# Optimization experiments

Hardware: AMD Instinct MI355X
Metric: run time of the kernel (lower is better)

## Reference

```python
import jax, jax.numpy as jnp
import numpy as np

N, E, H, L, T = 20000, 160000, 128, 4, 20


def _ln(x, g, b):
    m = jnp.mean(x, -1, keepdims=True)
    v = jnp.mean((x - m) ** 2, -1, keepdims=True)
    return (x - m) * jax.lax.rsqrt(v + 1e-5) * g + b


def _mlp(x, W1, b1, W2, b2, g, b):
    # Linear -> ReLU -> Linear -> LayerNorm, as in mlp_2layer
    h = jax.nn.relu(x @ W1 + b1)
    return _ln(h @ W2 + b2, g, b)


def setup_inputs() -> dict:
    key = jax.random.key(0)
    ks = iter(jax.random.split(key, 64))

    def W(shape):
        fan_in = shape[-2]
        return jax.random.normal(next(ks), shape, jnp.float32) * (fan_in ** -0.5)

    z = lambda s: jnp.zeros(s, jnp.float32)
    o = lambda s: jnp.ones(s, jnp.float32)

    inp = {
        'x': jax.random.normal(next(ks), (N, 12), jnp.float32),
        'edge_attr': jax.random.normal(next(ks), (E, 4), jnp.float32),
        'edge_index': jax.random.randint(next(ks), (2, E), 0, N),
        # node encoder (12 -> H)
        'Wn1': W((12, H)), 'bn1': z((H,)), 'Wn2': W((H, H)), 'bn2': z((H,)), 'gn_ln': o((H,)), 'bn_ln': z((H,)),
        # edge encoder (4 -> H)
        'We1': W((4, H)), 'be1': z((H,)), 'We2': W((H, H)), 'be2': z((H,)), 'ge_ln': o((H,)), 'be_ln': z((H,)),
        # stacked per-layer params: edge_mlp (4H -> H), node_mlp (3H -> H), global_mlp (3H -> H)
        'lEW1': W((L, 4 * H, H)), 'lEb1': z((L, H)), 'lEW2': W((L, H, H)), 'lEb2': z((L, H)), 'lEg': o((L, H)), 'lEbt': z((L, H)),
        'lVW1': W((L, 3 * H, H)), 'lVb1': z((L, H)), 'lVW2': W((L, H, H)), 'lVb2': z((L, H)), 'lVg': o((L, H)), 'lVbt': z((L, H)),
        'lGW1': W((L, 3 * H, H)), 'lGb1': z((L, H)), 'lGW2': W((L, H, H)), 'lGb2': z((L, H)), 'lGg': o((L, H)), 'lGbt': z((L, H)),
        # CNN output head: Conv1d(1->8,k=15,s=4) -> ReLU -> Conv1d(8->1,k=10,s=1)
        'c1w': jax.random.normal(next(ks), (8, 1, 15), jnp.float32) * 0.1, 'c1b': z((8,)),
        'c2w': jax.random.normal(next(ks), (1, 8, 10), jnp.float32) * 0.1, 'c2b': z((1,)),
    }
    return inp


def _forward(x, edge_attr, edge_index,
             Wn1, bn1, Wn2, bn2, gn_ln, bn_ln,
             We1, be1, We2, be2, ge_ln, be_ln,
             lEW1, lEb1, lEW2, lEb2, lEg, lEbt,
             lVW1, lVb1, lVW2, lVb2, lVg, lVbt,
             lGW1, lGb1, lGW2, lGb2, lGg, lGbt,
             c1w, c1b, c2w, c2b):
    senders = edge_index[0]
    receivers = edge_index[1]
    n_nodes = x.shape[0]
    n_edges = edge_attr.shape[0]

    x_v = _mlp(x, Wn1, bn1, Wn2, bn2, gn_ln, bn_ln)          # [N, H]
    x_e = _mlp(edge_attr, We1, be1, We2, be2, ge_ln, be_ln)  # [E, H]
    g = jnp.zeros((1, H), x_v.dtype)                          # B=1 global (no global inputs)

    def step(carry, p):
        x_v, x_e, g = carry
        (EW1, Eb1, EW2, Eb2, Eg, Ebt,
         VW1, Vb1, VW2, Vb2, Vg, Vbt,
         GW1, Gb1, GW2, Gb2, Gg, Gbt) = p
        # edge update: gather sender/receiver feats, concat with edge + global
        g_e = jnp.broadcast_to(g, (n_edges, H))
        edge_in = jnp.concatenate([x_v[senders], x_v[receivers], x_e, g_e], -1)  # [E, 4H]
        x_e = x_e + _mlp(edge_in, EW1, Eb1, EW2, Eb2, Eg, Ebt)
        # node update: sum-aggregate messages by receiver
        aggr = jax.ops.segment_sum(x_e, receivers, num_segments=n_nodes)  # [N, H]
        g_v = jnp.broadcast_to(g, (n_nodes, H))
        node_in = jnp.concatenate([x_v, aggr, g_v], -1)  # [N, 3H]
        x_v = x_v + _mlp(node_in, VW1, Vb1, VW2, Vb2, Vg, Vbt)
        # global update
        g_in = jnp.concatenate([jnp.sum(x_v, 0, keepdims=True), jnp.sum(x_e, 0, keepdims=True), g], -1)  # [1, 3H]
        g = g + _mlp(g_in, GW1, Gb1, GW2, Gb2, Gg, Gbt)
        return (x_v, x_e, g), None

    params = (lEW1, lEb1, lEW2, lEb2, lEg, lEbt,
              lVW1, lVb1, lVW2, lVb2, lVg, lVbt,
              lGW1, lGb1, lGW2, lGb2, lGg, lGbt)
    (x_v, x_e, g), _ = jax.lax.scan(step, (x_v, x_e, g), params)

    # CNN head over the H=128 feature axis -> [N, T]
    dn = ('NCH', 'OIH', 'NCH')
    h = x_v[:, None, :]  # [N, 1, 128]
    h = jax.lax.conv_general_dilated(h, c1w, (4,), 'VALID', dimension_numbers=dn)
    h = jax.nn.relu(h + c1b[None, :, None])  # [N, 8, 29]
    h = jax.lax.conv_general_dilated(h, c2w, (1,), 'VALID', dimension_numbers=dn) + c2b[None, :, None]
    return h[:, 0, :]  # [N, 20]


def reference(x, edge_attr, edge_index,
              Wn1, bn1, Wn2, bn2, gn_ln, bn_ln,
              We1, be1, We2, be2, ge_ln, be_ln,
              lEW1, lEb1, lEW2, lEb2, lEg, lEbt,
              lVW1, lVb1, lVW2, lVb2, lVg, lVbt,
              lGW1, lGb1, lGW2, lGb2, lGg, lGbt,
              c1w, c1b, c2w, c2b):
    return _forward(x, edge_attr, edge_index,
                    Wn1, bn1, Wn2, bn2, gn_ln, bn_ln,
                    We1, be1, We2, be2, ge_ln, be_ln,
                    lEW1, lEb1, lEW2, lEb2, lEg, lEbt,
                    lVW1, lVb1, lVW2, lVb2, lVg, lVbt,
                    lGW1, lGb1, lGW2, lGb2, lGg, lGbt,
                    c1w, c1b, c2w, c2b)
```

## Files before the change

kernel.cpp:

```cpp
#include <hip/hip_runtime.h>

#define NN 20000
#define NE 160000
#define HD 128
#define SA 136

typedef __attribute__((ext_vector_type(8))) short  bfrag;
typedef __attribute__((ext_vector_type(4))) short  s4v;
typedef __attribute__((ext_vector_type(4))) float  facc;
typedef __attribute__((ext_vector_type(4))) float  f4v;

__device__ __forceinline__ float bf2f(unsigned short u){
  union { unsigned int i; float f; } v; v.i = ((unsigned int)u) << 16; return v.f;
}
__device__ __forceinline__ unsigned short f2bf(float f){
  union { float f; unsigned int i; } v; v.f = f;
  unsigned int r = v.i + 0x7fffu + ((v.i >> 16) & 1u);
  return (unsigned short)(r >> 16);
}

__global__ void sentinel_kernel(float* out, float code){
  if (threadIdx.x < 32) out[threadIdx.x] = code;
}

__device__ __forceinline__ void gemm_tile(const short* Ab,
                                          const unsigned short* pk,
                                          int m0, int lane, facc acc[8]){
  const int q = lane >> 4, c = lane & 15;
  #pragma unroll
  for (int kt = 0; kt < 4; ++kt){
    bfrag a = *(const bfrag*)(Ab + (m0 + c) * SA + kt * 32 + q * 8);
    const bfrag* bp = (const bfrag*)pk + kt * 512 + lane;
    #pragma unroll
    for (int nt = 0; nt < 8; ++nt){
      acc[nt] = __builtin_amdgcn_mfma_f32_16x16x32_bf16(a, bp[nt * 64], acc[nt], 0, 0, 0);
    }
  }
}

__device__ __forceinline__ void gemm_tile_h(const short* Ab,
                                            const unsigned short* pk,
                                            int m0, int ntb, int lane, facc acc[4]){
  const int q = lane >> 4, c = lane & 15;
  #pragma unroll
  for (int kt = 0; kt < 4; ++kt){
    bfrag a = *(const bfrag*)(Ab + (m0 + c) * SA + kt * 32 + q * 8);
    const bfrag* bp = (const bfrag*)pk + kt * 512 + ntb * 64 + lane;
    #pragma unroll
    for (int nt = 0; nt < 4; ++nt){
      acc[nt] = __builtin_amdgcn_mfma_f32_16x16x32_bf16(a, bp[nt * 64], acc[nt], 0, 0, 0);
    }
  }
}

__global__ __launch_bounds__(256) void pack_all(
    const float* Wn2, const float* We2,
    const float* lEW1, const float* lEW2,
    const float* lVW1, const float* lVW2,
    unsigned short* packed)
{
  int job = blockIdx.x * 256 + threadIdx.x;
  int mat = job >> 12, r12 = job & 4095;
  int plane = r12 >> 11, r = r12 & 2047;
  int kt = r >> 9, nt = (r >> 6) & 7, lane = r & 63;
  const float* src;
  if (mat == 0) src = Wn2;
  else if (mat == 1) src = We2;
  else {
    int m2 = mat - 2, l = m2 / 7, t = m2 % 7;
    switch (t){
      case 0: src = lEW1 + ((size_t)l*512 +   0)*HD; break;
      case 1: src = lEW1 + ((size_t)l*512 + 128)*HD; break;
      case 2: src = lEW1 + ((size_t)l*512 + 256)*HD; break;
      case 3: src = lEW2 + (size_t)l*HD*HD;          break;
      case 4: src = lVW1 + ((size_t)l*384 +   0)*HD; break;
      case 5: src = lVW1 + ((size_t)l*384 + 128)*HD; break;
      default: src = lVW2 + (size_t)l*HD*HD;         break;
    }
  }
  int krow = kt*32 + (lane>>4)*8, col = nt*16 + (lane&15);
  unsigned short v[8];
  #pragma unroll
  for (int j = 0; j < 8; ++j){
    float w = src[(size_t)(krow + j)*HD + col];
    unsigned short h = f2bf(w);
    v[j] = plane ? f2bf(w - bf2f(h)) : h;
  }
  unsigned short* dst = packed + ((size_t)mat*2 + plane)*16384
                               + ((size_t)(kt*8+nt)*64 + lane)*8;
  #pragma unroll
  for (int j = 0; j < 8; ++j) dst[j] = v[j];
}

__global__ __launch_bounds__(128) void init_small(
    float* g, float* cbe, float* cbv, float* xvs, float* xes,
    const float* Eb1_0, const float* Vb1_0)
{
  int t = threadIdx.x;
  g[t] = 0.f; xvs[t] = 0.f; xes[t] = 0.f;
  cbe[t] = Eb1_0[t]; cbv[t] = Vb1_0[t];
}

__global__ __launch_bounds__(256) void zero_cnt(int* cnt){
  int i = blockIdx.x * 256 + threadIdx.x;
  if (i < NN) cnt[i] = 0;
}
__global__ __launch_bounds__(256) void hist_kernel(const int* eidx, int* cnt){
  int e = blockIdx.x * 256 + threadIdx.x;
  atomicAdd(&cnt[eidx[NE + e]], 1);
}
__global__ __launch_bounds__(1024) void scan_kernel(const int* cnt, int* base, int* ofs){
  __shared__ int wsum[16];
  int t = threadIdx.x, lane = t & 63;
  int vals[20]; int loc = 0;
  if (t < 1000){
    #pragma unroll
    for (int k = 0; k < 20; ++k){ vals[k] = cnt[t*20 + k]; loc += vals[k]; }
  }
  int inc = loc;
  #pragma unroll
  for (int d = 1; d < 64; d <<= 1){ int o = __shfl_up(inc, d); if (lane >= d) inc += o; }
  if (lane == 63) wsum[t >> 6] = inc;
  __syncthreads();
  if (t < 16){
    int v = wsum[t];
    #pragma unroll
    for (int d = 1; d < 16; d <<= 1){ int o = __shfl_up(v, d); if (t >= d) v += o; }
    wsum[t] = v;
  }
  __syncthreads();
  int woff = (t >= 64) ? wsum[(t >> 6) - 1] : 0;
  int run = woff + inc - loc;
  if (t < 1000){
    #pragma unroll
    for (int k = 0; k < 20; ++k){ base[t*20 + k] = run; ofs[t*20 + k] = run; run += vals[k]; }
  }
  if (t == 0) base[NN] = NE;
}
__global__ __launch_bounds__(256) void scatter_kernel(const int* eidx, int* ofs,
                                                      int* perm, int* ssid, int* srid){
  int e = blockIdx.x * 256 + threadIdx.x;
  int s = eidx[e], r = eidx[NE + e];
  int pos = atomicAdd(&ofs[r], 1);
  perm[pos] = e; ssid[pos] = s; srid[pos] = r;
}

__global__ __launch_bounds__(256) void enc_node(
    const float* x, const float* W1, const float* b1,
    const unsigned short* pkW2, const float* b2,
    const float* gl, const float* bl, float* xvf, int nrows)
{
  __shared__ float inb[64*12];
  __shared__ __align__(16) short Hh[64*SA];
  __shared__ __align__(16) short Hl[64*SA];
  int tid = threadIdx.x, r0 = blockIdx.x * 64;
  for (int j = tid; j < 64*12; j += 256){
    int rr = j / 12, k = j % 12, rg = r0 + rr;
    inb[j] = (rg < nrows) ? x[(size_t)rg*12 + k] : 0.f;
  }
  __syncthreads();
  {
    int cc = tid & 127;
    float w1c[12];
    #pragma unroll
    for (int k = 0; k < 12; ++k) w1c[k] = W1[k*HD + cc];
    float bb = b1[cc];
    for (int it = 0; it < 32; ++it){
      int rr = it*2 + (tid >> 7);
      float a = bb;
      #pragma unroll
      for (int k = 0; k < 12; ++k) a += inb[rr*12 + k] * w1c[k];
      float h = fmaxf(a, 0.f);
      unsigned short hh = f2bf(h);
      Hh[rr*SA + cc] = (short)hh;
      Hl[rr*SA + cc] = (short)f2bf(h - bf2f(hh));
    }
  }
  __syncthreads();
  int lane = tid & 63, q = lane >> 4, c = lane & 15, m0 = (tid >> 6) * 16;
  facc a2[8];
  #pragma unroll
  for (int nt = 0; nt < 8; ++nt) a2[nt] = (facc){0.f,0.f,0.f,0.f};
  gemm_tile(Hh, pkW2,         m0, lane, a2);
  gemm_tile(Hl, pkW2,         m0, lane, a2);
  gemm_tile(Hh, pkW2 + 16384, m0, lane, a2);
  #pragma unroll
  for (int i = 0; i < 4; ++i){
    int rl = m0 + q*4 + i, rg = r0 + rl;
    float vals[8], s = 0.f, ss = 0.f;
    #pragma unroll
    for (int nt = 0; nt < 8; ++nt){
      float v = a2[nt][i] + b2[nt*16 + c];
      vals[nt] = v; s += v; ss += v*v;
    }
    s += __shfl_xor(s,1); ss += __shfl_xor(ss,1);
    s += __shfl_xor(s,2); ss += __shfl_xor(ss,2);
    s += __shfl_xor(s,4); ss += __shfl_xor(ss,4);
    s += __shfl_xor(s,8); ss += __shfl_xor(ss,8);
    float mean = s * 0.0078125f;
    float var  = ss * 0.0078125f - mean*mean;
    float rs   = rsqrtf(var + 1e-5f);
    if (rg < nrows){
      #pragma unroll
      for (int nt = 0; nt < 8; ++nt){
        int col = nt*16 + c;
        xvf[(size_t)rg*HD + col] = (vals[nt]-mean)*rs*gl[col] + bl[col];
      }
    }
  }
}

__global__ __launch_bounds__(256) void enc_edge(
    const float* ea, const int* perm, const float* W1, const float* b1,
    const unsigned short* pkW2, const float* b2,
    const float* gl, const float* bl, unsigned short* xeb)
{
  __shared__ float inb[64*4];
  __shared__ __align__(16) short Hh[64*SA];
  __shared__ __align__(16) short Hl[64*SA];
  int tid = threadIdx.x, r0 = blockIdx.x * 64;
  {
    int rr = tid >> 2, k = tid & 3;
    int pe = perm[r0 + rr];
    inb[tid] = ea[(size_t)pe*4 + k];
  }
  __syncthreads();
  {
    int cc = tid & 127;
    float w0 = W1[0*HD+cc], w1 = W1[1*HD+cc], w2 = W1[2*HD+cc], w3 = W1[3*HD+cc];
    float bb = b1[cc];
    for (int it = 0; it < 32; ++it){
      int rr = it*2 + (tid >> 7);
      float a = bb + inb[rr*4+0]*w0 + inb[rr*4+1]*w1 + inb[rr*4+2]*w2 + inb[rr*4+3]*w3;
      float h = fmaxf(a, 0.f);
      unsigned short hh = f2bf(h);
      Hh[rr*SA + cc] = (short)hh;
      Hl[rr*SA + cc] = (short)f2bf(h - bf2f(hh));
    }
  }
  __syncthreads();
  int lane = tid & 63, q = lane >> 4, c = lane & 15, m0 = (tid >> 6) * 16;
  facc a2[8];
  #pragma unroll
  for (int nt = 0; nt < 8; ++nt) a2[nt] = (facc){0.f,0.f,0.f,0.f};
  gemm_tile(Hh, pkW2,         m0, lane, a2);
  gemm_tile(Hl, pkW2,         m0, lane, a2);
  gemm_tile(Hh, pkW2 + 16384, m0, lane, a2);
  #pragma unroll
  for (int i = 0; i < 4; ++i){
    int rl = m0 + q*4 + i, rg = r0 + rl;
    float vals[8], s = 0.f, ss = 0.f;
    #pragma unroll
    for (int nt = 0; nt < 8; ++nt){
      float v = a2[nt][i] + b2[nt*16 + c];
      vals[nt] = v; s += v; ss += v*v;
    }
    s += __shfl_xor(s,1); ss += __shfl_xor(ss,1);
    s += __shfl_xor(s,2); ss += __shfl_xor(ss,2);
    s += __shfl_xor(s,4); ss += __shfl_xor(ss,4);
    s += __shfl_xor(s,8); ss += __shfl_xor(ss,8);
    float mean = s * 0.0078125f;
    float var  = ss * 0.0078125f - mean*mean;
    float rs   = rsqrtf(var + 1e-5f);
    #pragma unroll
    for (int nt = 0; nt < 8; ++nt){
      int col = nt*16 + c;
      xeb[(size_t)rg*HD + col] = f2bf((vals[nt]-mean)*rs*gl[col] + bl[col]);
    }
  }
}

__global__ __launch_bounds__(512, 4) void pq_kernel(
    const float* xvf, const unsigned short* pkA, const unsigned short* pkB,
    unsigned short* P, unsigned short* Q, int nrows)
{
  __shared__ __align__(16) short Ah[64*SA];
  __shared__ __align__(16) short Al[64*SA];
  int tid = threadIdx.x, r0 = blockIdx.x * 64;
  for (int j = tid; j < 1024; j += 512){
    int rr = j >> 4, ch = j & 15, rg = r0 + rr;
    float v[8];
    if (rg < nrows){
      f4v a = *(const f4v*)(xvf + (size_t)rg*HD + ch*8);
      f4v b = *(const f4v*)(xvf + (size_t)rg*HD + ch*8 + 4);
      v[0]=a[0];v[1]=a[1];v[2]=a[2];v[3]=a[3];v[4]=b[0];v[5]=b[1];v[6]=b[2];v[7]=b[3];
    } else {
      #pragma unroll
      for (int k = 0; k < 8; ++k) v[k] = 0.f;
    }
    short* dh = Ah + rr*SA + ch*8;
    short* dl = Al + rr*SA + ch*8;
    #pragma unroll
    for (int k = 0; k < 8; ++k){
      unsigned short h = f2bf(v[k]);
      dh[k] = (short)h; dl[k] = (short)f2bf(v[k] - bf2f(h));
    }
  }
  __syncthreads();
  int lane = tid & 63, wq = tid >> 6, q = lane >> 4, c = lane & 15;
  int m0 = (wq & 3) * 16, ntb = (wq >> 2) * 4;
  facc ap[4], aq[4];
  #pragma unroll
  for (int nt = 0; nt < 4; ++nt){ ap[nt] = (facc){0.f,0.f,0.f,0.f}; aq[nt] = (facc){0.f,0.f,0.f,0.f}; }
  gemm_tile_h(Ah, pkA,         m0, ntb, lane, ap);
  gemm_tile_h(Al, pkA,         m0, ntb, lane, ap);
  gemm_tile_h(Ah, pkA + 16384, m0, ntb, lane, ap);
  gemm_tile_h(Ah, pkB,         m0, ntb, lane, aq);
  gemm_tile_h(Al, pkB,         m0, ntb, lane, aq);
  gemm_tile_h(Ah, pkB + 16384, m0, ntb, lane, aq);
  #pragma unroll
  for (int i = 0; i < 4; ++i){
    int rl = m0 + q*4 + i, rg = r0 + rl;
    if (rg < nrows){
      s4v pv, qv;
      #pragma unroll
      for (int nt = 0; nt < 4; ++nt){
        pv[nt] = (short)f2bf(ap[nt][i]);
        qv[nt] = (short)f2bf(aq[nt][i]);
      }
      *(s4v*)(P + (size_t)rg*HD + c*8 + ntb) = pv;
      *(s4v*)(Q + (size_t)rg*HD + c*8 + ntb) = qv;
    }
  }
}

__global__ __launch_bounds__(256) void edge_kernel(
    unsigned short* xeb, const int* ssid, const int* srid,
    const unsigned short* P, const unsigned short* Q, const float* cbe,
    const unsigned short* pkW1c, const unsigned short* pkW2,
    const float* Eb2, const float* Eg, const float* Ebt)
{
  __shared__ __align__(16) short Ab[64*SA];
  __shared__ __align__(16) short Hh[64*SA];
  __shared__ __align__(16) short Hl[64*SA];
  __shared__ int sidx[64], ridx[64];
  int tid = threadIdx.x, e0 = blockIdx.x * 64;
  for (int j = tid; j < 1024; j += 256){
    int rr = j >> 4, ch = j & 15;
    *(bfrag*)(Ab + rr*SA + ch*8) = *(const bfrag*)(xeb + (size_t)(e0+rr)*HD + ch*8);
  }
  if (tid < 64){ sidx[tid] = ssid[e0+tid]; ridx[tid] = srid[e0+tid]; }
  __syncthreads();
  int lane = tid & 63, q = lane >> 4, c = lane & 15, m0 = (tid >> 6) * 16;
  float cb[8];
  #pragma unroll
  for (int nt = 0; nt < 8; ++nt) cb[nt] = cbe[nt*16 + c];
  float pg[4][8];
  #pragma unroll
  for (int i = 0; i < 4; ++i){
    int rl = m0 + q*4 + i;
    bfrag ps = *(const bfrag*)(P + (size_t)sidx[rl]*HD + c*8);
    bfrag qr = *(const bfrag*)(Q + (size_t)ridx[rl]*HD + c*8);
    #pragma unroll
    for (int nt = 0; nt < 8; ++nt)
      pg[i][nt] = bf2f((unsigned short)ps[nt]) + bf2f((unsigned short)qr[nt]) + cb[nt];
  }
  facc acc[8];
  #pragma unroll
  for (int nt = 0; nt < 8; ++nt) acc[nt] = (facc){0.f,0.f,0.f,0.f};
  gemm_tile(Ab, pkW1c,         m0, lane, acc);
  gemm_tile(Ab, pkW1c + 16384, m0, lane, acc);
  #pragma unroll
  for (int i = 0; i < 4; ++i){
    int rl = m0 + q*4 + i;
    #pragma unroll
    for (int nt = 0; nt < 8; ++nt){
      int col = nt*16 + c;
      float h = fmaxf(acc[nt][i] + pg[i][nt], 0.f);
      unsigned short hh = f2bf(h);
      Hh[rl*SA + col] = (short)hh;
      Hl[rl*SA + col] = (short)f2bf(h - bf2f(hh));
    }
  }
  __syncthreads();
  facc a2[8];
  #pragma unroll
  for (int nt = 0; nt < 8; ++nt) a2[nt] = (facc){0.f,0.f,0.f,0.f};
  gemm_tile(Hh, pkW2,         m0, lane, a2);
  gemm_tile(Hl, pkW2,         m0, lane, a2);
  gemm_tile(Hh, pkW2 + 16384, m0, lane, a2);
  #pragma unroll
  for (int i = 0; i < 4; ++i){
    int rl = m0 + q*4 + i, eg = e0 + rl;
    float vals[8], s = 0.f, ss = 0.f;
    #pragma unroll
    for (int nt = 0; nt < 8; ++nt){
      float v = a2[nt][i] + Eb2[nt*16 + c];
      vals[nt] = v; s += v; ss += v*v;
    }
    s += __shfl_xor(s,1); ss += __shfl_xor(ss,1);
    s += __shfl_xor(s,2); ss += __shfl_xor(ss,2);
    s += __shfl_xor(s,4); ss += __shfl_xor(ss,4);
    s += __shfl_xor(s,8); ss += __shfl_xor(ss,8);
    float mean = s * 0.0078125f;
    float var  = ss * 0.0078125f - mean*mean;
    float rs   = rsqrtf(var + 1e-5f);
    #pragma unroll
    for (int nt = 0; nt < 8; ++nt){
      int col = nt*16 + c;
      float o = (vals[nt]-mean)*rs*Eg[col] + Ebt[col];
      float nv = bf2f((unsigned short)Ab[rl*SA + col]) + o;
      xeb[(size_t)eg*HD + col] = f2bf(nv);
    }
  }
}

__global__ __launch_bounds__(512, 4) void node_kernel(
    float* xvf, const unsigned short* xeb, const int* base, const float* cbv,
    const unsigned short* pkW1a, const unsigned short* pkW1b, const unsigned short* pkW2,
    const float* Vb2, const float* Vg, const float* Vbt,
    float* xv_sum, float* xes, int do_xes, int nrows)
{
  __shared__ __align__(16) short Avh[64*SA];
  __shared__ __align__(16) short Avl[64*SA];
  __shared__ __align__(16) short Agh[64*SA];
  __shared__ __align__(16) short Agl[64*SA];
  __shared__ float red[128];
  __shared__ float lnS[128], lnSS[128];
  int tid = threadIdx.x, r0 = blockIdx.x * 64;
  int lane = tid & 63, wq = tid >> 6;
  if (tid < 128) red[tid] = 0.f;
  __syncthreads();
  for (int j = tid; j < 1024; j += 512){
    int rr = j >> 4, ch = j & 15, rg = r0 + rr;
    float v[8];
    if (rg < nrows){
      f4v a = *(const f4v*)(xvf + (size_t)rg*HD + ch*8);
      f4v b = *(const f4v*)(xvf + (size_t)rg*HD + ch*8 + 4);
      v[0]=a[0];v[1]=a[1];v[2]=a[2];v[3]=a[3];v[4]=b[0];v[5]=b[1];v[6]=b[2];v[7]=b[3];
    } else {
      #pragma unroll
      for (int k = 0; k < 8; ++k) v[k] = 0.f;
    }
    short *dvh = Avh + rr*SA + ch*8, *dvl = Avl + rr*SA + ch*8;
    #pragma unroll
    for (int k = 0; k < 8; ++k){
      unsigned short h1 = f2bf(v[k]);
      dvh[k] = (short)h1; dvl[k] = (short)f2bf(v[k] - bf2f(h1));
    }
  }
  float xp0 = 0.f, xp1 = 0.f;
  for (int j = 0; j < 8; ++j){
    int rl = wq*8 + j, rg = r0 + rl;
    float s0 = 0.f, s1 = 0.f;
    if (rg < nrows){
      int b0 = base[rg], b1 = base[rg + 1];
      int e = b0;
      for (; e + 1 < b1; e += 2){
        unsigned int u0 = *(const unsigned int*)(xeb + (size_t)e*HD + lane*2);
        unsigned int u1 = *(const unsigned int*)(xeb + (size_t)(e+1)*HD + lane*2);
        s0 += bf2f((unsigned short)(u0 & 0xffffu)) + bf2f((unsigned short)(u1 & 0xffffu));
        s1 += bf2f((unsigned short)(u0 >> 16))     + bf2f((unsigned short)(u1 >> 16));
      }
      if (e < b1){
        unsigned int u0 = *(const unsigned int*)(xeb + (size_t)e*HD + lane*2);
        s0 += bf2f((unsigned short)(u0 & 0xffffu));
        s1 += bf2f((unsigned short)(u0 >> 16));
      }
    }
    unsigned short h0 = f2bf(s0), h1 = f2bf(s1);
    unsigned short l0 = f2bf(s0 - bf2f(h0)), l1 = f2bf(s1 - bf2f(h1));
    *(unsigned int*)(Agh + rl*SA + 2*lane) = ((unsigned int)h1 << 16) | h0;
    *(unsigned int*)(Agl + rl*SA + 2*lane) = ((unsigned int)l1 << 16) | l0;
    xp0 += s0; xp1 += s1;
  }
  if (do_xes){
    atomicAdd(&red[lane*2],     xp0);
    atomicAdd(&red[lane*2 + 1], xp1);
  }
  __syncthreads();
  if (do_xes && tid < 128) atomicAdd(&xes[tid], red[tid]);
  int q = lane >> 4, c = lane & 15;
  int m0 = (wq & 3) * 16, ntb = (wq >> 2) * 4, half = wq >> 2;
  facc acc[4];
  #pragma unroll
  for (int nt = 0; nt < 4; ++nt) acc[nt] = (facc){0.f,0.f,0.f,0.f};
  gemm_tile_h(Avh, pkW1a,         m0, ntb, lane, acc);
  gemm_tile_h(Avl, pkW1a,         m0, ntb, lane, acc);
  gemm_tile_h(Avh, pkW1a + 16384, m0, ntb, lane, acc);
  gemm_tile_h(Agh, pkW1b,         m0, ntb, lane, acc);
  gemm_tile_h(Agl, pkW1b,         m0, ntb, lane, acc);
  gemm_tile_h(Agh, pkW1b + 16384, m0, ntb, lane, acc);
  __syncthreads();
  #pragma unroll
  for (int i = 0; i < 4; ++i){
    int rl = m0 + q*4 + i;
    #pragma unroll
    for (int nt = 0; nt < 4; ++nt){
      int col = (ntb + nt)*16 + c;
      float h = fmaxf(acc[nt][i] + cbv[col], 0.f);
      unsigned short hh = f2bf(h);
      Avh[rl*SA + col] = (short)hh;
      Avl[rl*SA + col] = (short)f2bf(h - bf2f(hh));
    }
  }
  __syncthreads();
  facc a2[4];
  #pragma unroll
  for (int nt = 0; nt < 4; ++nt) a2[nt] = (facc){0.f,0.f,0.f,0.f};
  gemm_tile_h(Avh, pkW2,         m0, ntb, lane, a2);
  gemm_tile_h(Avl, pkW2,         m0, ntb, lane, a2);
  gemm_tile_h(Avh, pkW2 + 16384, m0, ntb, lane, a2);
  float vals[4][4], myS[4], mySS[4];
  #pragma unroll
  for (int i = 0; i < 4; ++i){
    int rl = m0 + q*4 + i;
    float s = 0.f, ss = 0.f;
    #pragma unroll
    for (int nt = 0; nt < 4; ++nt){
      float v = a2[nt][i] + Vb2[(ntb + nt)*16 + c];
      vals[i][nt] = v; s += v; ss += v*v;
    }
    s += __shfl_xor(s,1); ss += __shfl_xor(ss,1);
    s += __shfl_xor(s,2); ss += __shfl_xor(ss,2);
    s += __shfl_xor(s,4); ss += __shfl_xor(ss,4);
    s += __shfl_xor(s,8); ss += __shfl_xor(ss,8);
    myS[i] = s; mySS[i] = ss;
    if (c == 0){ lnS[rl*2 + half] = s; lnSS[rl*2 + half] = ss; }
  }
  __syncthreads();
  float csum[4] = {0.f,0.f,0.f,0.f};
  #pragma unroll
  for (int i = 0; i < 4; ++i){
    int rl = m0 + q*4 + i, rg = r0 + rl;
    float sT  = myS[i]  + lnS[rl*2 + (half^1)];
    float ssT = mySS[i] + lnSS[rl*2 + (half^1)];
    float mean = sT * 0.0078125f;
    float var  = ssT * 0.0078125f - mean*mean;
    float rs   = rsqrtf(var + 1e-5f);
    if (rg < nrows){
      #pragma unroll
      for (int nt = 0; nt < 4; ++nt){
        int col = (ntb + nt)*16 + c;
        float o = (vals[i][nt]-mean)*rs*Vg[col] + Vbt[col];
        size_t gi = (size_t)rg*HD + col;
        float nv = xvf[gi] + o;
        xvf[gi] = nv;
        csum[nt] += nv;
      }
    }
  }
  #pragma unroll
  for (int nt = 0; nt < 4; ++nt){
    float v = csum[nt]; v += __shfl_xor(v,16); v += __shfl_xor(v,32);
    if (q == 0) atomicAdd(&xv_sum[(ntb + nt)*16 + c], v);
  }
}

__global__ __launch_bounds__(1024) void g_kernel(
    float* xvs, float* xes, float* g,
    const float* GW1, const float* Gb1, const float* GW2, const float* Gb2,
    const float* Gg, const float* Gbt,
    float* cbe, float* cbv,
    const float* EW1n, const float* Eb1n, const float* VW1n, const float* Vb1n)
{
  __shared__ float gin[384], h1[128], gn[128], red[4];
  __shared__ float partA[8][128], partB[8][128];
  int tid = threadIdx.x, t = tid & 127, kk = tid >> 7;
  if (tid < 384) gin[tid] = (tid < 128) ? xvs[tid] : (tid < 256) ? xes[tid-128] : g[tid-256];
  __syncthreads();
  {
    float a = 0.f;
    for (int k = kk*48; k < kk*48 + 48; ++k) a += gin[k] * GW1[(size_t)k*HD + t];
    partA[kk][t] = a;
  }
  __syncthreads();
  if (kk == 0){
    float a = Gb1[t];
    #pragma unroll
    for (int i = 0; i < 8; ++i) a += partA[i][t];
    h1[t] = fmaxf(a, 0.f);
  }
  __syncthreads();
  {
    float o = 0.f;
    for (int k = kk*16; k < kk*16 + 16; ++k) o += h1[k] * GW2[(size_t)k*HD + t];
    partA[kk][t] = o;
  }
  __syncthreads();
  float oo = 0.f;
  if (kk == 0){
    oo = Gb2[t];
    #pragma unroll
    for (int i = 0; i < 8; ++i) oo += partA[i][t];
  }
  __syncthreads();
  if (tid < 128){
    float s = oo;
    #pragma unroll
    for (int d = 1; d < 64; d <<= 1) s += __shfl_xor(s, d);
    if ((tid & 63) == 0) red[tid >> 6] = s;
  }
  __syncthreads();
  float mean = (red[0] + red[1]) * 0.0078125f;
  if (tid < 128){
    float dd = oo - mean;
    float v = dd * dd;
    #pragma unroll
    for (int d = 1; d < 64; d <<= 1) v += __shfl_xor(v, d);
    if ((tid & 63) == 0) red[2 + (tid >> 6)] = v;
  }
  __syncthreads();
  if (tid < 128){
    float rs = rsqrtf((red[2] + red[3]) * 0.0078125f + 1e-5f);
    float gnv = g[tid] + (oo - mean)*rs*Gg[tid] + Gbt[tid];
    g[tid] = gnv; gn[tid] = gnv;
    xvs[tid] = 0.f; xes[tid] = 0.f;
  }
  __syncthreads();
  {
    float ce = 0.f, cv = 0.f;
    for (int k = kk*16; k < kk*16 + 16; ++k){
      ce += gn[k] * EW1n[(size_t)k*HD + t];
      cv += gn[k] * VW1n[(size_t)k*HD + t];
    }
    partA[kk][t] = ce; partB[kk][t] = cv;
  }
  __syncthreads();
  if (kk == 0){
    float ce = Eb1n[t], cv = Vb1n[t];
    #pragma unroll
    for (int i = 0; i < 8; ++i){ ce += partA[i][t]; cv += partB[i][t]; }
    cbe[t] = ce; cbv[t] = cv;
  }
}

__global__ __launch_bounds__(256) void decoder_kernel(
    const float* xv, const float* c1w, const float* c1b,
    const float* c2w, const float* c2b, float* out)
{
  __shared__ float xl[4][128];
  __shared__ float hl[4][232];
  __shared__ float w1[120], b1[8], w2[80];
  __shared__ float b2s;
  int tid = threadIdx.x, nl = tid >> 6, t = tid & 63;
  int n = blockIdx.x * 4 + nl;
  if (tid < 120) w1[tid] = c1w[tid];
  else if (tid < 128) b1[tid - 120] = c1b[tid - 120];
  else if (tid < 208) w2[tid - 128] = c2w[tid - 128];
  else if (tid == 208) b2s = c2b[0];
  xl[nl][t]      = xv[(size_t)n*HD + t];
  xl[nl][t + 64] = xv[(size_t)n*HD + 64 + t];
  __syncthreads();
  for (int j = t; j < 232; j += 64){
    int ch = j / 29, pp = j % 29;
    float a = b1[ch];
    #pragma unroll
    for (int u = 0; u < 15; ++u) a += xl[nl][4*pp + u] * w1[ch*15 + u];
    hl[nl][j] = fmaxf(a, 0.f);
  }
  __syncthreads();
  if (t < 20){
    float o = b2s;
    #pragma unroll
    for (int ch = 0; ch < 8; ++ch)
      #pragma unroll
      for (int u = 0; u < 10; ++u)
        o += hl[nl][ch*29 + t + u] * w2[ch*10 + u];
    out[(size_t)n*20 + t] = o;
  }
}

extern "C" void kernel_launch(void* const* d_in, const int* in_sizes, int n_in,
                              void* d_out, int out_size, void* d_ws, size_t ws_size,
                              hipStream_t stream)
{
  const float* x    = (const float*)d_in[0];
  const float* ea   = (const float*)d_in[1];
  const int*   eidx = (const int*)d_in[2];
  const float* Wn1  = (const float*)d_in[3];  const float* bn1  = (const float*)d_in[4];
  const float* Wn2  = (const float*)d_in[5];  const float* bn2  = (const float*)d_in[6];
  const float* gnln = (const float*)d_in[7];  const float* bnln = (const float*)d_in[8];
  const float* We1  = (const float*)d_in[9];  const float* be1  = (const float*)d_in[10];
  const float* We2  = (const float*)d_in[11]; const float* be2  = (const float*)d_in[12];
  const float* geln = (const float*)d_in[13]; const float* beln = (const float*)d_in[14];
  const float* lEW1 = (const float*)d_in[15]; const float* lEb1 = (const float*)d_in[16];
  const float* lEW2 = (const float*)d_in[17]; const float* lEb2 = (const float*)d_in[18];
  const float* lEg  = (const float*)d_in[19]; const float* lEbt = (const float*)d_in[20];
  const float* lVW1 = (const float*)d_in[21]; const float* lVb1 = (const float*)d_in[22];
  const float* lVW2 = (const float*)d_in[23]; const float* lVb2 = (const float*)d_in[24];
  const float* lVg  = (const float*)d_in[25]; const float* lVbt = (const float*)d_in[26];
  const float* lGW1 = (const float*)d_in[27]; const float* lGb1 = (const float*)d_in[28];
  const float* lGW2 = (const float*)d_in[29]; const float* lGb2 = (const float*)d_in[30];
  const float* lGg  = (const float*)d_in[31]; const float* lGbt = (const float*)d_in[32];
  const float* c1w  = (const float*)d_in[33]; const float* c1b  = (const float*)d_in[34];
  const float* c2w  = (const float*)d_in[35]; const float* c2b  = (const float*)d_in[36];

  char* ws = (char*)d_ws;
  size_t off = 0;
  auto alloc = [&](size_t b){ size_t o = off; off += (b + 255) & ~(size_t)255; return o; };
  unsigned short* pk   = (unsigned short*)(ws + alloc((size_t)30*2*16384*2));
  float*          g    = (float*)(ws + alloc(512));
  float*          cbe  = (float*)(ws + alloc(512));
  float*          cbv  = (float*)(ws + alloc(512));
  float*          xvs  = (float*)(ws + alloc(512));
  float*          xes  = (float*)(ws + alloc(512));
  float*          xvf  = (float*)(ws + alloc((size_t)NN*HD*4));
  unsigned short* P    = (unsigned short*)(ws + alloc((size_t)NN*HD*2));
  unsigned short* Q    = (unsigned short*)(ws + alloc((size_t)NN*HD*2));
  unsigned short* xeb  = (unsigned short*)(ws + alloc((size_t)NE*HD*2));
  int*            cnt  = (int*)(ws + alloc((size_t)NN*4));
  int*            bse  = (int*)(ws + alloc((size_t)(NN+1)*4));
  int*            ofs  = (int*)(ws + alloc((size_t)NN*4));
  int*            perm = (int*)(ws + alloc((size_t)NE*4));
  int*            ssid = (int*)(ws + alloc((size_t)NE*4));
  int*            srid = (int*)(ws + alloc((size_t)NE*4));

  if (ws_size < off){
    sentinel_kernel<<<1, 32, 0, stream>>>((float*)d_out, 20000.f + (float)(ws_size >> 20));
    return;
  }

  auto slot = [&](int m){ return pk + (size_t)m * 32768; };

  pack_all<<<480, 256, 0, stream>>>(Wn2, We2, lEW1, lEW2, lVW1, lVW2, pk);
  init_small<<<1, 128, 0, stream>>>(g, cbe, cbv, xvs, xes, lEb1, lVb1);
  zero_cnt<<<(NN + 255)/256, 256, 0, stream>>>(cnt);
  hist_kernel<<<NE/256, 256, 0, stream>>>(eidx, cnt);
  scan_kernel<<<1, 1024, 0, stream>>>(cnt, bse, ofs);
  scatter_kernel<<<NE/256, 256, 0, stream>>>(eidx, ofs, perm, ssid, srid);

  enc_node<<<(NN + 63)/64, 256, 0, stream>>>(x, Wn1, bn1, slot(0), bn2, gnln, bnln, xvf, NN);
  enc_edge<<<NE/64, 256, 0, stream>>>(ea, perm, We1, be1, slot(1), be2, geln, beln, xeb);

  for (int l = 0; l < 4; ++l){
    int m = 2 + 7*l;
    pq_kernel<<<(NN + 63)/64, 512, 0, stream>>>(xvf, slot(m+0), slot(m+1), P, Q, NN);
    edge_kernel<<<NE/64, 256, 0, stream>>>(xeb, ssid, srid, P, Q, cbe,
        slot(m+2), slot(m+3),
        lEb2 + (size_t)l*HD, lEg + (size_t)l*HD, lEbt + (size_t)l*HD);
    node_kernel<<<(NN + 63)/64, 512, 0, stream>>>(xvf, xeb, bse, cbv,
        slot(m+4), slot(m+5), slot(m+6),
        lVb2 + (size_t)l*HD, lVg + (size_t)l*HD, lVbt + (size_t)l*HD,
        xvs, xes, (l < 3) ? 1 : 0, NN);
    if (l < 3){
      g_kernel<<<1, 1024, 0, stream>>>(xvs, xes, g,
          lGW1 + (size_t)l*384*HD, lGb1 + (size_t)l*HD,
          lGW2 + (size_t)l*HD*HD, lGb2 + (size_t)l*HD,
          lGg + (size_t)l*HD, lGbt + (size_t)l*HD,
          cbe, cbv,
          lEW1 + ((size_t)(l+1)*512 + 384)*HD, lEb1 + (size_t)(l+1)*HD,
          lVW1 + ((size_t)(l+1)*384 + 256)*HD, lVb1 + (size_t)(l+1)*HD);
    }
  }
  decoder_kernel<<<NN/4, 256, 0, stream>>>(xvf, c1w, c1b, c2w, c2b, (float*)d_out);

  hipError_t e = hipGetLastError();
  if (e != hipSuccess){
    sentinel_kernel<<<1, 32, 0, stream>>>((float*)d_out, 10000.f + (float)e);
  }
  (void)in_sizes; (void)n_in; (void)out_size;
}
```

Measured before the change: 848.1 us.

## Split edge kernel column tiles across 8 waves and reuse shared buffers

The edge kernel now runs 512 threads per block, with each wave computing half of the output columns (4 n-tiles) for its 16-row slice via gemm_tile_h. This halves per-thread accumulator registers and adds more waves per block. The residual is kept in registers so the Ab buffer can hold the hidden high part, which removes the Hh buffer and cuts LDS per block. LayerNorm statistics are combined across the two column halves through shared memory, which costs extra __syncthreads barriers.

```diff
diff --git a/kernel.cpp b/kernel.cpp
--- a/kernel.cpp
+++ b/kernel.cpp
@@ -324,83 +324,106 @@
   }
 }
 
-__global__ __launch_bounds__(256) void edge_kernel(
+__global__ __launch_bounds__(512, 4) void edge_kernel(
     unsigned short* xeb, const int* ssid, const int* srid,
     const unsigned short* P, const unsigned short* Q, const float* cbe,
     const unsigned short* pkW1c, const unsigned short* pkW2,
     const float* Eb2, const float* Eg, const float* Ebt)
 {
   __shared__ __align__(16) short Ab[64*SA];
-  __shared__ __align__(16) short Hh[64*SA];
   __shared__ __align__(16) short Hl[64*SA];
   __shared__ int sidx[64], ridx[64];
+  __shared__ float lnS[128], lnSS[128];
   int tid = threadIdx.x, e0 = blockIdx.x * 64;
-  for (int j = tid; j < 1024; j += 256){
+  for (int j = tid; j < 1024; j += 512){
     int rr = j >> 4, ch = j & 15;
     *(bfrag*)(Ab + rr*SA + ch*8) = *(const bfrag*)(xeb + (size_t)(e0+rr)*HD + ch*8);
   }
   if (tid < 64){ sidx[tid] = ssid[e0+tid]; ridx[tid] = srid[e0+tid]; }
   __syncthreads();
-  int lane = tid & 63, q = lane >> 4, c = lane & 15, m0 = (tid >> 6) * 16;
-  float cb[8];
-  #pragma unroll
-  for (int nt = 0; nt < 8; ++nt) cb[nt] = cbe[nt*16 + c];
-  float pg[4][8];
+  int lane = tid & 63, wq = tid >> 6, q = lane >> 4, c = lane & 15;
+  int m0 = (wq & 3) * 16, ntb = (wq >> 2) * 4, half = wq >> 2;
+  unsigned int rres[4][2];
   #pragma unroll
   for (int i = 0; i < 4; ++i){
     int rl = m0 + q*4 + i;
-    bfrag ps = *(const bfrag*)(P + (size_t)sidx[rl]*HD + c*8);
-    bfrag qr = *(const bfrag*)(Q + (size_t)ridx[rl]*HD + c*8);
-    #pragma unroll
-    for (int nt = 0; nt < 8; ++nt)
+    #pragma unroll
+    for (int p2 = 0; p2 < 2; ++p2){
+      unsigned short a0 = (unsigned short)Ab[rl*SA + (ntb + 2*p2    )*16 + c];
+      unsigned short a1 = (unsigned short)Ab[rl*SA + (ntb + 2*p2 + 1)*16 + c];
+      rres[i][p2] = ((unsigned int)a1 << 16) | a0;
+    }
+  }
+  float cb[4];
+  #pragma unroll
+  for (int nt = 0; nt < 4; ++nt) cb[nt] = cbe[(ntb + nt)*16 + c];
+  float pg[4][4];
+  #pragma unroll
+  for (int i = 0; i < 4; ++i){
+    int rl = m0 + q*4 + i;
+    s4v ps = *(const s4v*)(P + (size_t)sidx[rl]*HD + c*8 + ntb);
+    s4v qr = *(const s4v*)(Q + (size_t)ridx[rl]*HD + c*8 + ntb);
+    #pragma unroll
+    for (int nt = 0; nt < 4; ++nt)
       pg[i][nt] = bf2f((unsigned short)ps[nt]) + bf2f((unsigned short)qr[nt]) + cb[nt];
   }
-  facc acc[8];
-  #pragma unroll
-  for (int nt = 0; nt < 8; ++nt) acc[nt] = (facc){0.f,0.f,0.f,0.f};
-  gemm_tile(Ab, pkW1c,         m0, lane, acc);
-  gemm_tile(Ab, pkW1c + 16384, m0, lane, acc);
+  facc acc[4];
+  #pragma unroll
+  for (int nt = 0; nt < 4; ++nt) acc[nt] = (facc){0.f,0.f,0.f,0.f};
+  gemm_tile_h(Ab, pkW1c,         m0, ntb, lane, acc);
+  gemm_tile_h(Ab, pkW1c + 16384, m0, ntb, lane, acc);
+  __syncthreads();
   #pragma unroll
   for (int i = 0; i < 4; ++i){
     int rl = m0 + q*4 + i;
     #pragma unroll
-    for (int nt = 0; nt < 8; ++nt){
-      int col = nt*16 + c;
+    for (int nt = 0; nt < 4; ++nt){
+      int col = (ntb + nt)*16 + c;
       float h = fmaxf(acc[nt][i] + pg[i][nt], 0.f);
       unsigned short hh = f2bf(h);
-      Hh[rl*SA + col] = (short)hh;
+      Ab[rl*SA + col] = (short)hh;
       Hl[rl*SA + col] = (short)f2bf(h - bf2f(hh));
     }
   }
   __syncthreads();
-  facc a2[8];
-  #pragma unroll
-  for (int nt = 0; nt < 8; ++nt) a2[nt] = (facc){0.f,0.f,0.f,0.f};
-  gemm_tile(Hh, pkW2,         m0, lane, a2);
-  gemm_tile(Hl, pkW2,         m0, lane, a2);
-  gemm_tile(Hh, pkW2 + 16384, m0, lane, a2);
-  #pragma unroll
-  for (int i = 0; i < 4; ++i){
-    int rl = m0 + q*4 + i, eg = e0 + rl;
-    float vals[8], s = 0.f, ss = 0.f;
-    #pragma unroll
-    for (int nt = 0; nt < 8; ++nt){
-      float v = a2[nt][i] + Eb2[nt*16 + c];
-      vals[nt] = v; s += v; ss += v*v;
+  facc a2[4];
+  #pragma unroll
+  for (int nt = 0; nt < 4; ++nt) a2[nt] = (facc){0.f,0.f,0.f,0.f};
+  gemm_tile_h(Ab, pkW2,         m0, ntb, lane, a2);
+  gemm_tile_h(Hl, pkW2,         m0, ntb, lane, a2);
+  gemm_tile_h(Ab, pkW2 + 16384, m0, ntb, lane, a2);
+  float vals[4][4], myS[4], mySS[4];
+  #pragma unroll
+  for (int i = 0; i < 4; ++i){
+    int rl = m0 + q*4 + i;
+    float s = 0.f, ss = 0.f;
+    #pragma unroll
+    for (int nt = 0; nt < 4; ++nt){
+      float v = a2[nt][i] + Eb2[(ntb + nt)*16 + c];
+      vals[i][nt] = v; s += v; ss += v*v;
     }
     s += __shfl_xor(s,1); ss += __shfl_xor(ss,1);
     s += __shfl_xor(s,2); ss += __shfl_xor(ss,2);
     s += __shfl_xor(s,4); ss += __shfl_xor(ss,4);
     s += __shfl_xor(s,8); ss += __shfl_xor(ss,8);
-    float mean = s * 0.0078125f;
-    float var  = ss * 0.0078125f - mean*mean;
+    myS[i] = s; mySS[i] = ss;
+    if (c == 0){ lnS[rl*2 + half] = s; lnSS[rl*2 + half] = ss; }
+  }
+  __syncthreads();
+  #pragma unroll
+  for (int i = 0; i < 4; ++i){
+    int rl = m0 + q*4 + i, eg = e0 + rl;
+    float sT  = myS[i]  + lnS[rl*2 + (half^1)];
+    float ssT = mySS[i] + lnSS[rl*2 + (half^1)];
+    float mean = sT * 0.0078125f;
+    float var  = ssT * 0.0078125f - mean*mean;
     float rs   = rsqrtf(var + 1e-5f);
     #pragma unroll
-    for (int nt = 0; nt < 8; ++nt){
-      int col = nt*16 + c;
-      float o = (vals[nt]-mean)*rs*Eg[col] + Ebt[col];
-      float nv = bf2f((unsigned short)Ab[rl*SA + col]) + o;
-      xeb[(size_t)eg*HD + col] = f2bf(nv);
+    for (int nt = 0; nt < 4; ++nt){
+      int col = (ntb + nt)*16 + c;
+      float o = (vals[i][nt]-mean)*rs*Eg[col] + Ebt[col];
+      float rv = bf2f((unsigned short)(rres[i][nt >> 1] >> ((nt & 1)*16)));
+      xeb[(size_t)eg*HD + col] = f2bf(rv + o);
     }
   }
 }
@@ -726,7 +749,7 @@
   for (int l = 0; l < 4; ++l){
     int m = 2 + 7*l;
     pq_kernel<<<(NN + 63)/64, 512, 0, stream>>>(xvf, slot(m+0), slot(m+1), P, Q, NN);
-    edge_kernel<<<NE/64, 256, 0, stream>>>(xeb, ssid, srid, P, Q, cbe,
+    edge_kernel<<<NE/64, 512, 0, stream>>>(xeb, ssid, srid, P, Q, cbe,
         slot(m+2), slot(m+3),
         lEb2 + (size_t)l*HD, lEg + (size_t)l*HD, lEbt + (size_t)l*HD);
     node_kernel<<<(NN + 63)/64, 512, 0, stream>>>(xvf, xeb, bse, cbv,
```

Measured after the change: 833.4 us. About the same (-1.7%).
